# Optimization experiments

Hardware: AMD Instinct MI355X
Metric: run time of the kernel (lower is better)

Reference implementation:

```python
import jax, jax.numpy as jnp
import numpy as np

B, N, H = 512, 100, 768
I = 2 * H  # intermediate_dim default = hidden_dim * 2
NUM_ANS = 16
MAX_ANS = 15
LN_EPS = 1e-5


def setup_inputs() -> dict:
    key = jax.random.key(0)
    ks = jax.random.split(key, 7)
    s = 0.02
    return {
        "v_emb": jax.random.normal(ks[0], (B, N, H), dtype=jnp.float32),
        "W1": jax.random.normal(ks[1], (H, I), dtype=jnp.float32) * s,
        "b1": jax.random.normal(ks[2], (I,), dtype=jnp.float32) * s,
        "gamma": jnp.ones((I,), dtype=jnp.float32),
        "beta": jnp.zeros((I,), dtype=jnp.float32),
        "W2": jax.random.normal(ks[3], (I, 1), dtype=jnp.float32) * s,
        "b2": jax.random.normal(ks[4], (1,), dtype=jnp.float32) * s,
    }


def reference(v_emb, W1, b1, gamma, beta, W2, b2):
    # Linear -> GELU (exact/erf, torch nn.GELU default) -> LayerNorm -> Linear
    h = jnp.einsum("bnh,hi->bni", v_emb, W1) + b1            # [B,N,I]
    h = jax.nn.gelu(h, approximate=False)
    mu = jnp.mean(h, axis=-1, keepdims=True)
    var = jnp.mean(jnp.square(h - mu), axis=-1, keepdims=True)
    h = (h - mu) * jax.lax.rsqrt(var + LN_EPS) * gamma + beta
    scores = jnp.einsum("bni,io->bno", h, W2) + b2           # [B,N,1]
    scores = jax.nn.sigmoid(scores)                           # sigmoid=True branch
    pred = jnp.sum(scores, axis=1)                            # [B,1]
    # pred_to_logits: vectorized round + clamp + one-hot scatter
    # str(int(round(p))) in {'0'..'15'} -> that id; negative -> 0; overflow -> max_ans
    aid = jnp.clip(jnp.round(pred[:, 0]).astype(jnp.int32), 0, MAX_ANS)
    logits = jax.nn.one_hot(aid, NUM_ANS, dtype=scores.dtype)  # [B,16]
    # original returns dict: scores, final_attention_map (==scores), pred, logits
    return scores, pred, logits
```

## Files before the change

kernel.cpp:

```cpp
#include <hip/hip_runtime.h>
#include <hip/hip_bf16.h>
#include <cstdint>
#include <cstddef>

#define BB   512
#define NN   100
#define HH   768
#define II   1536
#define MM   (BB*NN)

typedef __bf16 bf16;
typedef __bf16 bf16x4 __attribute__((ext_vector_type(4)));
typedef __bf16 bf16x8 __attribute__((ext_vector_type(8)));
typedef float  f32x4  __attribute__((ext_vector_type(4)));

__device__ __forceinline__ void gld_lds16(const void* g, void* l) {
    __builtin_amdgcn_global_load_lds(
        (const __attribute__((address_space(1))) void*)g,
        (__attribute__((address_space(3))) void*)l, 16, 0, 0);
}

template <int PAT>
__device__ __forceinline__ float swz_add(float x) {
    return x + __int_as_float(
        __builtin_amdgcn_ds_swizzle(__float_as_int(x), PAT));
}
__device__ __forceinline__ float red16(float x) {
    x = swz_add<0x041F>(x);
    x = swz_add<0x081F>(x);
    x = swz_add<0x101F>(x);
    x = swz_add<0x201F>(x);
    return x;
}

__device__ __forceinline__ float fast_gelu(float x) {
    const float ax = fabsf(x) * 0.70710678118654752f;
    const float t  = __builtin_amdgcn_rcpf(fmaf(0.3275911f, ax, 1.0f));
    float p = fmaf(1.061405429f, t, -1.453152027f);
    p = fmaf(p, t, 1.421413741f);
    p = fmaf(p, t, -0.284496736f);
    p = fmaf(p, t, 0.254829592f);
    p = p * t;
    const float e    = __expf(-ax * ax);
    const float erfa = fmaf(-p, e, 1.0f);
    const float erfx = copysignf(erfa, x);
    return 0.5f * x * (1.0f + erfx);
}

__global__ __launch_bounds__(256) void prep_kernel(
    const float* __restrict__ W1, const float* __restrict__ gamma,
    const float* __restrict__ beta, const float* __restrict__ W2,
    const float* __restrict__ b2, const float* __restrict__ A,
    bf16* __restrict__ Wp, float* __restrict__ gw, float* __restrict__ scal,
    bf16* __restrict__ Apk)
{
    const int bid = blockIdx.x, tid = threadIdx.x;
    if (bid >= 290) {
        const size_t base = (size_t)(bid - 290) * 4096 + tid * 4;
        #pragma unroll
        for (int it = 0; it < 4; ++it) {
            const size_t i = base + it * 1024;
            float4 v = *(const float4*)&A[i];
            bf16x4 o = { (bf16)v.x, (bf16)v.y, (bf16)v.z, (bf16)v.w };
            *(bf16x4*)&Apk[i] = o;
        }
    } else if (bid < 288) {
        __shared__ bf16 Ts[64 * 72];
        const int kt = bid % 12, nt = bid / 12;
        const int k0 = kt * 64, n0 = nt * 64;
        #pragma unroll
        for (int it = 0; it < 4; ++it) {
            const int idx = it * 256 + tid;
            const int r   = idx >> 4;
            const int c4  = idx & 15;
            float4 v = *(const float4*)&W1[(size_t)(k0 + r) * II + n0 + c4*4];
            Ts[(c4*4 + 0) * 72 + r] = (bf16)v.x;
            Ts[(c4*4 + 1) * 72 + r] = (bf16)v.y;
            Ts[(c4*4 + 2) * 72 + r] = (bf16)v.z;
            Ts[(c4*4 + 3) * 72 + r] = (bf16)v.w;
        }
        __syncthreads();
        #pragma unroll
        for (int it = 0; it < 2; ++it) {
            const int idx = it * 256 + tid;
            const int nr  = idx >> 3;
            const int kc  = idx & 7;
            *(bf16x8*)&Wp[(size_t)(n0 + nr) * HH + k0 + kc*8]
                = *(const bf16x8*)&Ts[nr * 72 + kc*8];
        }
    } else if (bid == 288) {
        for (int j = tid; j < II; j += 256)
            gw[j] = gamma[j] * W2[j];
    } else {
        float s1 = 0.f, s2 = 0.f;
        for (int j = tid; j < II; j += 256) {
            float w2 = W2[j];
            s1 += gamma[j] * w2;
            s2 += beta[j]  * w2;
        }
        #pragma unroll
        for (int off = 32; off; off >>= 1) {
            s1 += __shfl_down(s1, off, 64);
            s2 += __shfl_down(s2, off, 64);
        }
        __shared__ float a1[4], a2[4];
        int lane = tid & 63, w = tid >> 6;
        if (lane == 0) { a1[w] = s1; a2[w] = s2; }
        __syncthreads();
        if (tid == 0) {
            scal[0] = a1[0] + a1[1] + a1[2] + a1[3];
            scal[1] = a2[0] + a2[1] + a2[2] + a2[3] + b2[0];
        }
    }
}

__global__ __launch_bounds__(256) void gemm_part(
    const bf16* __restrict__ Apk, const bf16* __restrict__ Wp,
    const float* __restrict__ b1, const float* __restrict__ gw,
    float* __restrict__ part)
{
    __shared__ bf16 As[128 * 64];
    __shared__ bf16 Bs[128 * 64];

    const int tid  = threadIdx.x;
    const int lin  = (blockIdx.x % 8) * 600 + blockIdx.x / 8;
    const int mb   = lin / 12;
    const int nb   = lin % 12;
    const int lane = tid & 63;
    const int w    = tid >> 6;
    const int wm   = w >> 1;
    const int wn   = w & 1;
    const int m15  = lane & 15;
    const int q    = lane >> 4;
    const int row0 = mb * 128;

    const int rsub  = tid >> 3;
    const int kg    = (tid & 7) ^ (rsub & 7);
    const int lbase = tid * 8;

    const bf16* aP = Apk + (size_t)(row0    + rsub) * HH + kg * 8;
    const bf16* bP = Wp  + (size_t)(nb*128 + rsub) * HH + kg * 8;

    f32x4 acc[4][4] = {};

    for (int kt = 0; kt < 12; ++kt) {
        #pragma unroll
        for (int it = 0; it < 4; ++it) {
            gld_lds16(aP + (size_t)it * 32 * HH, &As[lbase + it * 2048]);
            gld_lds16(bP + (size_t)it * 32 * HH, &Bs[lbase + it * 2048]);
        }
        asm volatile("s_waitcnt vmcnt(0)" ::: "memory");
        __syncthreads();

        #pragma unroll
        for (int kb = 0; kb < 2; ++kb) {
            const int swz = (((kb * 4 + q) ^ (m15 & 7)) * 8);
            bf16x8 af[4], bfr[4];
            #pragma unroll
            for (int mt = 0; mt < 4; ++mt)
                af[mt] = *(const bf16x8*)&As[(wm*64 + mt*16 + m15) * 64 + swz];
            #pragma unroll
            for (int nt = 0; nt < 4; ++nt)
                bfr[nt] = *(const bf16x8*)&Bs[(wn*64 + nt*16 + m15) * 64 + swz];
            #pragma unroll
            for (int mt = 0; mt < 4; ++mt)
                #pragma unroll
                for (int nt = 0; nt < 4; ++nt)
                    acc[mt][nt] = __builtin_amdgcn_mfma_f32_16x16x32_bf16(
                        af[mt], bfr[nt], acc[mt][nt], 0, 0, 0);
        }
        __syncthreads();
        aP += 64; bP += 64;
    }

    float* sred = (float*)As;

    float bv[4], gv[4];
    #pragma unroll
    for (int nt = 0; nt < 4; ++nt) {
        const int col = nb*128 + wn*64 + nt*16 + m15;
        bv[nt] = b1[col];
        gv[nt] = gw[col];
    }

    #pragma unroll
    for (int mt = 0; mt < 4; ++mt) {
        #pragma unroll
        for (int r = 0; r < 4; ++r) {
            float x0 = 0.f, x1 = 0.f, x2 = 0.f;
            #pragma unroll
            for (int nt = 0; nt < 4; ++nt) {
                float g = fast_gelu(acc[mt][nt][r] + bv[nt]);
                x0 += g; x1 += g * g; x2 += g * gv[nt];
            }
            x0 = red16(x0); x1 = red16(x1); x2 = red16(x2);
            if (m15 == 0) {
                const int rl = wm*64 + mt*16 + q*4 + r;
                sred[wn*384 + rl*3 + 0] = x0;
                sred[wn*384 + rl*3 + 1] = x1;
                sred[wn*384 + rl*3 + 2] = x2;
            }
        }
    }
    __syncthreads();

    if (tid < 128) {
        const size_t rg = (size_t)row0 + tid;
        #pragma unroll
        for (int s = 0; s < 3; ++s)
            part[(size_t)s * 12 * MM + (size_t)nb * MM + rg]
                = sred[0*384 + tid*3 + s] + sred[1*384 + tid*3 + s];
    }
}

__global__ __launch_bounds__(128) void score_pred(
    const float* __restrict__ part, const float* __restrict__ scal,
    float* __restrict__ o_scores, float* __restrict__ o_pred,
    float* __restrict__ o_logits)
{
    const int b = blockIdx.x, t = threadIdx.x;
    float s = 0.f;
    if (t < NN) {
        const size_t row = (size_t)b * NN + t;
        float Sh = 0.f, Shh = 0.f, Shg = 0.f;
        #pragma unroll
        for (int j = 0; j < 12; ++j) {
            Sh  += part[(size_t)0*12*MM + (size_t)j*MM + row];
            Shh += part[(size_t)1*12*MM + (size_t)j*MM + row];
            Shg += part[(size_t)2*12*MM + (size_t)j*MM + row];
        }
        const float mu   = Sh * (1.0f / II);
        const float var  = Shh * (1.0f / II) - mu * mu;
        const float rstd = rsqrtf(var + 1e-5f);
        const float z    = rstd * (Shg - mu * scal[0]) + scal[1];
        s = 1.0f / (1.0f + __expf(-z));
        o_scores[row] = s;
    }
    float v = s;
    #pragma unroll
    for (int off = 32; off; off >>= 1) v += __shfl_down(v, off, 64);
    __shared__ float ssum[2];
    const int lane = t & 63, w = t >> 6;
    if (lane == 0) ssum[w] = v;
    __syncthreads();
    const float p = ssum[0] + ssum[1];
    if (t == 0) o_pred[b] = p;
    if (t < 16) {
        int aid = (int)rintf(p);
        aid = aid < 0 ? 0 : (aid > 15 ? 15 : aid);
        o_logits[b * 16 + t] = (t == aid) ? 1.0f : 0.0f;
    }
}

extern "C" void kernel_launch(void* const* d_in, const int* in_sizes, int n_in,
                              void* d_out, int out_size, void* d_ws, size_t ws_size,
                              hipStream_t stream)
{
    const float* v_emb = (const float*)d_in[0];
    const float* W1    = (const float*)d_in[1];
    const float* b1    = (const float*)d_in[2];
    const float* gamma = (const float*)d_in[3];
    const float* beta  = (const float*)d_in[4];
    const float* W2    = (const float*)d_in[5];
    const float* b2    = (const float*)d_in[6];

    char* ws = (char*)d_ws;
    size_t off = 0;
    bf16*  Wp   = (bf16*)(ws + off);  off += (size_t)II * HH * 2;
    float* gw   = (float*)(ws + off); off += (size_t)II * 4;
    float* scal = (float*)(ws + off); off += 256;
    float* part = (float*)(ws + off); off += (size_t)MM * 36 * 4;
    bf16*  Apk  = (bf16*)(ws + off);  off += (size_t)MM * HH * 2;

    float* out       = (float*)d_out;
    float* o_scores  = out;
    float* o_pred    = out + MM;
    float* o_logits  = out + MM + BB;

    hipLaunchKernelGGL(prep_kernel, dim3(290 + 9600), dim3(256), 0, stream,
                       W1, gamma, beta, W2, b2, v_emb, Wp, gw, scal, Apk);
    hipLaunchKernelGGL(gemm_part, dim3((MM / 128) * 12), dim3(256),
                       0, stream, Apk, Wp, b1, gw, part);
    hipLaunchKernelGGL(score_pred, dim3(BB), dim3(128), 0, stream,
                       part, scal, o_scores, o_pred, o_logits);
}
```

Measured before the change: 428.1 us.

## Fuse fp32-to-bf16 activation conversion into GEMM A-tile loading

Removes the separate pass that converted the full activation matrix to bf16 in workspace. The GEMM now loads fp32 A tiles into registers, prefetching one k-step ahead, then converts them and stores them to shared memory. This avoids a large HBM write and re-read. In exchange, every N-block re-reads fp32 A, doubling A bytes per tile, and registers are used for the prefetch.

```diff
diff --git a/kernel.cpp b/kernel.cpp
--- a/kernel.cpp
+++ b/kernel.cpp
@@ -50,21 +50,11 @@
 __global__ __launch_bounds__(256) void prep_kernel(
     const float* __restrict__ W1, const float* __restrict__ gamma,
     const float* __restrict__ beta, const float* __restrict__ W2,
-    const float* __restrict__ b2, const float* __restrict__ A,
-    bf16* __restrict__ Wp, float* __restrict__ gw, float* __restrict__ scal,
-    bf16* __restrict__ Apk)
+    const float* __restrict__ b2,
+    bf16* __restrict__ Wp, float* __restrict__ gw, float* __restrict__ scal)
 {
     const int bid = blockIdx.x, tid = threadIdx.x;
-    if (bid >= 290) {
-        const size_t base = (size_t)(bid - 290) * 4096 + tid * 4;
-        #pragma unroll
-        for (int it = 0; it < 4; ++it) {
-            const size_t i = base + it * 1024;
-            float4 v = *(const float4*)&A[i];
-            bf16x4 o = { (bf16)v.x, (bf16)v.y, (bf16)v.z, (bf16)v.w };
-            *(bf16x4*)&Apk[i] = o;
-        }
-    } else if (bid < 288) {
+    if (bid < 288) {
         __shared__ bf16 Ts[64 * 72];
         const int kt = bid % 12, nt = bid / 12;
         const int k0 = kt * 64, n0 = nt * 64;
@@ -115,7 +105,7 @@
 }
 
 __global__ __launch_bounds__(256) void gemm_part(
-    const bf16* __restrict__ Apk, const bf16* __restrict__ Wp,
+    const float* __restrict__ Af, const bf16* __restrict__ Wp,
     const float* __restrict__ b1, const float* __restrict__ gw,
     float* __restrict__ part)
 {
@@ -138,19 +128,42 @@
     const int kg    = (tid & 7) ^ (rsub & 7);
     const int lbase = tid * 8;
 
-    const bf16* aP = Apk + (size_t)(row0    + rsub) * HH + kg * 8;
-    const bf16* bP = Wp  + (size_t)(nb*128 + rsub) * HH + kg * 8;
+    const float* aP = Af + (size_t)(row0    + rsub) * HH + kg * 8;
+    const bf16*  bP = Wp + (size_t)(nb*128 + rsub) * HH + kg * 8;
+
+    float4 av[4][2];
+    #pragma unroll
+    for (int it = 0; it < 4; ++it) {
+        const float* s = aP + (size_t)it * 32 * HH;
+        av[it][0] = *(const float4*)s;
+        av[it][1] = *(const float4*)(s + 4);
+    }
 
     f32x4 acc[4][4] = {};
 
     for (int kt = 0; kt < 12; ++kt) {
         #pragma unroll
+        for (int it = 0; it < 4; ++it)
+            gld_lds16(bP + (size_t)it * 32 * HH, &Bs[lbase + it * 2048]);
+        #pragma unroll
         for (int it = 0; it < 4; ++it) {
-            gld_lds16(aP + (size_t)it * 32 * HH, &As[lbase + it * 2048]);
-            gld_lds16(bP + (size_t)it * 32 * HH, &Bs[lbase + it * 2048]);
+            const float4 v0 = av[it][0], v1 = av[it][1];
+            bf16x8 o = { (bf16)v0.x, (bf16)v0.y, (bf16)v0.z, (bf16)v0.w,
+                         (bf16)v1.x, (bf16)v1.y, (bf16)v1.z, (bf16)v1.w };
+            *(bf16x8*)&As[lbase + it * 2048] = o;
         }
         asm volatile("s_waitcnt vmcnt(0)" ::: "memory");
         __syncthreads();
+
+        aP += 64;
+        if (kt < 11) {
+            #pragma unroll
+            for (int it = 0; it < 4; ++it) {
+                const float* s = aP + (size_t)it * 32 * HH;
+                av[it][0] = *(const float4*)s;
+                av[it][1] = *(const float4*)(s + 4);
+            }
+        }
 
         #pragma unroll
         for (int kb = 0; kb < 2; ++kb) {
@@ -170,7 +183,7 @@
                         af[mt], bfr[nt], acc[mt][nt], 0, 0, 0);
         }
         __syncthreads();
-        aP += 64; bP += 64;
+        bP += 64;
     }
 
     float* sred = (float*)As;
@@ -270,17 +283,16 @@
     float* gw   = (float*)(ws + off); off += (size_t)II * 4;
     float* scal = (float*)(ws + off); off += 256;
     float* part = (float*)(ws + off); off += (size_t)MM * 36 * 4;
-    bf16*  Apk  = (bf16*)(ws + off);  off += (size_t)MM * HH * 2;
 
     float* out       = (float*)d_out;
     float* o_scores  = out;
     float* o_pred    = out + MM;
     float* o_logits  = out + MM + BB;
 
-    hipLaunchKernelGGL(prep_kernel, dim3(290 + 9600), dim3(256), 0, stream,
-                       W1, gamma, beta, W2, b2, v_emb, Wp, gw, scal, Apk);
+    hipLaunchKernelGGL(prep_kernel, dim3(290), dim3(256), 0, stream,
+                       W1, gamma, beta, W2, b2, Wp, gw, scal);
     hipLaunchKernelGGL(gemm_part, dim3((MM / 128) * 12), dim3(256),
-                       0, stream, Apk, Wp, b1, gw, part);
+                       0, stream, v_emb, Wp, b1, gw, part);
     hipLaunchKernelGGL(score_pred, dim3(BB), dim3(128), 0, stream,
                        part, scal, o_scores, o_pred, o_logits);
 }
```

Measured after the change: 487.6 us. 1.14x slower.
